# Kernel tuning notes

Measured on AMD Instinct MI355X. Metric: run time of the kernel, lower is better.

Reference implementation:

```python
import jax, jax.numpy as jnp
import numpy as np

# irreps_in  = 128x0 + 64x1   (128 scalars, 64 vectors) -> dim 320
# irreps_out = 128x0 + 64x1 ; irreps_with_gates = (128+64)x0 + 64x1
B = 8192          # batch (nodes)
N0, N1 = 128, 64  # input multiplicities: scalars, vectors
NS, NV = 128, 64  # output scalars, gated vectors (NV gates appended to scalars)

_eps = np.zeros((3, 3, 3), np.float32)
_eps[0, 1, 2] = _eps[1, 2, 0] = _eps[2, 0, 1] = 1.0
_eps[0, 2, 1] = _eps[2, 1, 0] = _eps[1, 0, 2] = -1.0
EPS = jnp.asarray(_eps)  # Levi-Civita, used for the 1x1->1 CG path


def setup_inputs() -> dict:
    key = jax.random.key(0)
    ks = jax.random.split(key, 5)
    x = jax.random.normal(ks[0], (B, N0 + 3 * N1), jnp.float32)
    # fully-connected (uvw) path weights of the tensor square
    w000 = jax.random.normal(ks[1], (N0, N0, NS + NV), jnp.float32)
    w110 = jax.random.normal(ks[2], (N1, N1, NS + NV), jnp.float32)
    w011 = jax.random.normal(ks[3], (N0, N1, NV), jnp.float32)
    w111 = jax.random.normal(ks[4], (N1, N1, NV), jnp.float32)
    return {"x": x, "w000": w000, "w110": w110, "w011": w011, "w111": w111}


def reference(x, w000, w110, w011, w111):
    x0 = x[:, :N0]                        # [B, N0] scalars
    x1 = x[:, N0:].reshape(-1, N1, 3)     # [B, N1, 3] vectors

    inv_sqrt2 = 1.0 / np.sqrt(2.0)

    # ---- tensor square, scalar (l=0) outputs: NS scalars + NV gates ----
    s000 = jnp.einsum('bu,bv,uvw->bw', x0, x0, w000) * (1.0 / N0)
    dots = jnp.einsum('bui,bvi->buv', x1, x1) * (1.0 / np.sqrt(3.0))
    s110 = jnp.einsum('buv,uvw->bw', dots, w110) * (1.0 / N1)
    scalars = (s000 + s110) * inv_sqrt2   # [B, NS+NV], avg over 2 paths

    # ---- tensor square, vector (l=1) outputs: NV vectors ----
    v011 = jnp.einsum('bu,bvi,uvw->bwi', x0, x1, w011) * (1.0 / np.sqrt(N0 * N1))
    v111 = jnp.einsum('ijk,bui,bvj,uvw->bwk', EPS, x1, x1, w111) * (inv_sqrt2 / N1)
    vecs = (v011 + v111) * inv_sqrt2      # [B, NV, 3]

    # ---- e3nn.nn.Gate ----
    s_out = jax.nn.silu(scalars[:, :NS])            # act_scalars on true scalars
    g = jax.nn.sigmoid(scalars[:, NS:])             # act_gates on NV gate scalars
    v_out = vecs * g[:, :, None]                    # gate the non-scalar irreps

    return jnp.concatenate([s_out, v_out.reshape(v_out.shape[0], -1)], axis=1)
```

## Files before the change

### kernel.cpp

```cpp
#include <hip/hip_runtime.h>
#include <cstdint>

static constexpr int B_  = 8192;
static constexpr int NW_ = 192;

typedef __attribute__((ext_vector_type(8))) _Float16 h8v;
typedef __attribute__((ext_vector_type(2))) _Float16 h2v;
typedef __attribute__((ext_vector_type(4))) float f4v;
typedef __attribute__((ext_vector_type(2))) float f2v;
typedef __attribute__((ext_vector_type(4))) unsigned u4v;
typedef __attribute__((ext_vector_type(2))) unsigned u2v;

#define DI __device__ __forceinline__

DI h2v uh(unsigned u) { return __builtin_bit_cast(h2v, u); }
DI unsigned hu(h2v h) { return __builtin_bit_cast(unsigned, h); }
DI h2v hsplat(unsigned short bits) {
  _Float16 v = __builtin_bit_cast(_Float16, bits);
  h2v t; t.x = v; t.y = v; return t;
}
DI unsigned hpack(float lo, float hi) {
  h2v t; t.x = (_Float16)lo; t.y = (_Float16)hi;
  return __builtin_bit_cast(unsigned, t);
}
DI short f2h_bits(float f) { return __builtin_bit_cast(short, (_Float16)f); }

DI f4v mfma16h(h8v a, h8v b, f4v c) {
  return __builtin_amdgcn_mfma_f32_16x16x32_f16(a, b, c, 0, 0, 0);
}

static constexpr unsigned PK_BU0 = 606436u;
static constexpr unsigned PK_BV0 = 1030628u;
static constexpr unsigned PK_BU2 = 4u;
static constexpr unsigned PK_BV2 = 20u;
DI int tab2(unsigned pack, int blk) { return (int)((pack >> (2 * blk)) & 3u); }

__global__ void prep_all(const float* __restrict__ w000, const float* __restrict__ w110,
                         const float* __restrict__ w011, const float* __restrict__ w111,
                         short* __restrict__ wsc, short* __restrict__ wve) {
  __shared__ unsigned short T[32][200];
  const int t = threadIdx.x;
  const int bi = blockIdx.x;
  const float s000 = 1.0f / (128.0f * 1.41421356237f);
  const float s110 = 1.0f / (64.0f * 2.44948974968f);
  const float sv   = 1.0f / 128.0f;

  if (bi < 416) {
    const int s = bi;
    const float* W; int dim; float scale; int blk, ik, bu, bv;
    if (s < 320) {
      blk = s >> 5; ik = s & 31;
      bu = tab2(PK_BU0, blk); bv = tab2(PK_BV0, blk);
      W = w000; dim = 128; scale = s000;
    } else {
      int sp = s - 320; blk = sp >> 5; ik = sp & 31;
      bu = tab2(PK_BU2, blk); bv = tab2(PK_BV2, blk);
      W = w110; dim = 64; scale = s110;
    }
    const int u = bu * 32 + ik;
    const int v = t >> 3, l8 = t & 7;
    float a[24];
    const float* pA = W + ((size_t)(u * dim) + bv * 32 + v) * 192 + l8 * 24;
#pragma unroll
    for (int jj = 0; jj < 6; ++jj) {
      f4v x4 = *(const f4v*)(pA + jj * 4);
      a[jj * 4] = x4.x; a[jj * 4 + 1] = x4.y; a[jj * 4 + 2] = x4.z; a[jj * 4 + 3] = x4.w;
    }
    if (bu != bv) {
      const float* pB = W + ((size_t)((bv * 32 + v)) * dim + u) * 192 + l8 * 24;
#pragma unroll
      for (int jj = 0; jj < 6; ++jj) {
        f4v x4 = *(const f4v*)(pB + jj * 4);
        a[jj * 4] += x4.x; a[jj * 4 + 1] += x4.y; a[jj * 4 + 2] += x4.z; a[jj * 4 + 3] += x4.w;
      }
    }
    unsigned o[12];
#pragma unroll
    for (int i = 0; i < 12; ++i) o[i] = hpack(a[2 * i] * scale, a[2 * i + 1] * scale);
#pragma unroll
    for (int i = 0; i < 3; ++i)
      *(u4v*)(&T[v][l8 * 24 + i * 8]) = u4v{o[4 * i], o[4 * i + 1], o[4 * i + 2], o[4 * i + 3]};
    __syncthreads();
    short* dst = wsc + (size_t)s * 6144;
#pragma unroll
    for (int k = 0; k < 3; ++k) {
      const int unit = t * 3 + k;
      const int F = unit >> 6, lane = unit & 63;
      const int n = F * 16 + (lane & 15);
      const int vr = (lane >> 4) * 8;
      short oo[8];
#pragma unroll
      for (int j = 0; j < 8; ++j) oo[j] = (short)T[vr + j][n];
      *(h8v*)(dst + F * 512 + lane * 8) = *(h8v*)oo;
    }
  } else {
    const int s = bi - 416;
    if (s < 256) {
      const int k32 = t >> 3, l8 = t & 7;
      const float* p = w011 + ((size_t)(s * 32 + k32)) * 64 + l8 * 8;
      f4v x0_ = *(const f4v*)p, x1_ = *(const f4v*)(p + 4);
      u4v o{hpack(x0_.x * sv, x0_.y * sv), hpack(x0_.z * sv, x0_.w * sv),
            hpack(x1_.x * sv, x1_.y * sv), hpack(x1_.z * sv, x1_.w * sv)};
      *(u4v*)(&T[k32][l8 * 8]) = o;
    } else {
      const int sp = s - 256;
      const int blk = sp >> 5, ik = sp & 31;
      const int bu = tab2(PK_BU2, blk), bv = tab2(PK_BV2, blk);
      const int u = bu * 32 + ik;
      const int v = t >> 3, l8 = t & 7;
      float a[8];
      const float* pA = w111 + ((size_t)(u * 64) + bv * 32 + v) * 64 + l8 * 8;
      f4v x0_ = *(const f4v*)pA, x1_ = *(const f4v*)(pA + 4);
      a[0] = x0_.x; a[1] = x0_.y; a[2] = x0_.z; a[3] = x0_.w;
      a[4] = x1_.x; a[5] = x1_.y; a[6] = x1_.z; a[7] = x1_.w;
      if (bu != bv) {
        const float* pB = w111 + ((size_t)((bv * 32 + v)) * 64 + u) * 64 + l8 * 8;
        f4v y0 = *(const f4v*)pB, y1 = *(const f4v*)(pB + 4);
        a[0] -= y0.x; a[1] -= y0.y; a[2] -= y0.z; a[3] -= y0.w;
        a[4] -= y1.x; a[5] -= y1.y; a[6] -= y1.z; a[7] -= y1.w;
      }
      u4v o{hpack(a[0] * sv, a[1] * sv), hpack(a[2] * sv, a[3] * sv),
            hpack(a[4] * sv, a[5] * sv), hpack(a[6] * sv, a[7] * sv)};
      *(u4v*)(&T[v][l8 * 8]) = o;
    }
    __syncthreads();
    const int nf = t >> 6, lane = t & 63;
    const int n = nf * 16 + (lane & 15);
    const int vr = (lane >> 4) * 8;
    short oo[8];
#pragma unroll
    for (int j = 0; j < 8; ++j) oo[j] = (short)T[vr + j][n];
    *(h8v*)(wve + (size_t)s * 2048 + nf * 512 + lane * 8) = *(h8v*)oo;
  }
}

#define X0H_STRIDE 136
#define X1_STRIDE  200

DI void stage_x32w(const float* __restrict__ x, int b0,
                   unsigned short* X0H, unsigned short* X1) {
  const int t = threadIdx.x;
  const int row = t >> 4, l16 = t & 15;
  const float* src = x + (size_t)(b0 + row) * 320;
  f4v v0 = *(const f4v*)(src + l16 * 8);
  f4v v1 = *(const f4v*)(src + l16 * 8 + 4);
  u4v o{hpack(v0.x, v0.y), hpack(v0.z, v0.w), hpack(v1.x, v1.y), hpack(v1.z, v1.w)};
  *(u4v*)(&X0H[row * X0H_STRIDE + l16 * 8]) = o;
  float buf[12];
  f4v a0 = *(const f4v*)(src + 128 + l16 * 12);
  f4v a1 = *(const f4v*)(src + 128 + l16 * 12 + 4);
  f4v a2 = *(const f4v*)(src + 128 + l16 * 12 + 8);
  buf[0] = a0.x; buf[1] = a0.y; buf[2] = a0.z; buf[3] = a0.w;
  buf[4] = a1.x; buf[5] = a1.y; buf[6] = a1.z; buf[7] = a1.w;
  buf[8] = a2.x; buf[9] = a2.y; buf[10] = a2.z; buf[11] = a2.w;
#pragma unroll
  for (int i = 0; i < 3; ++i) {
    u2v w2{hpack(buf[i], buf[3 + i]), hpack(buf[6 + i], buf[9 + i])};
    *(u2v*)(&X1[row * X1_STRIDE + i * 64 + l16 * 4]) = w2;
  }
}

DI void loadB6(h8v* dst, const short* __restrict__ p) {
#pragma unroll
  for (int nf = 0; nf < 6; ++nf) dst[nf] = *(const h8v*)(p + nf * 512);
}
DI void loadB2(h8v* dst, const short* __restrict__ p) {
  dst[0] = *(const h8v*)p;
  dst[1] = *(const h8v*)(p + 512);
}

__global__ __launch_bounds__(512, 2)
void gemm_fused(const float* __restrict__ x, const short* __restrict__ wsc,
                const short* __restrict__ wve, float* __restrict__ out) {
  __shared__ unsigned short X0H[32 * X0H_STRIDE];
  __shared__ unsigned short X1[32 * X1_STRIDE];
  __shared__ f4v dump[4][12][64];
  __shared__ float G[32][64];
  const int b0 = blockIdx.x * 32;

  stage_x32w(x, b0, X0H, X1);
  __syncthreads();

  const int t0 = threadIdx.x;
  const int w = t0 >> 6, lane = t0 & 63;
  const bool isvec = w >= 4;
  const int nh = w & 1, kh = (w >> 1) & 1;
  const int q = lane >> 4, r = lane & 15, q8 = q * 8;

  f4v acc[12];
#pragma unroll
  for (int i = 0; i < 12; ++i) acc[i] = f4v{0.f, 0.f, 0.f, 0.f};

  if (!isvec) {
    const unsigned short* x0f[2];
    const unsigned short* x1f[2];
#pragma unroll
    for (int f = 0; f < 2; ++f) {
      x0f[f] = &X0H[(f * 16 + r) * X0H_STRIDE];
      x1f[f] = &X1[(f * 16 + r) * X1_STRIDE];
    }

    {
      const int s0 = kh * 160;
      const short* wp = wsc + ((size_t)s0 * 12 + nh * 6) * 512 + lane * 8;
      u4v pv[2]; pv[0] = u4v{0, 0, 0, 0}; pv[1] = u4v{0, 0, 0, 0};
      int bu32 = 0;
      h8v b[4][6];
      loadB6(b[0], wp); loadB6(b[1], wp + 6144); loadB6(b[2], wp + 12288);
      for (int t4 = 0; t4 < 40; ++t4) {
#pragma unroll
        for (int uu = 0; uu < 4; ++uu) {
          const int t = t4 * 4 + uu;
          if (t < 157) loadB6(b[(uu + 3) & 3], wp + (size_t)(t + 3) * 6144);
          const int s = s0 + t;
          const int ik = s & 31;
          if (t == 0 || ik == 0) {
            const int blk = s >> 5;
            const int bv32 = tab2(PK_BV0, blk) * 32;
            bu32 = tab2(PK_BU0, blk) * 32;
            pv[0] = *(const u4v*)(x0f[0] + bv32 + q8);
            pv[1] = *(const u4v*)(x0f[1] + bv32 + q8);
          }
          h8v a[2];
#pragma unroll
          for (int f = 0; f < 2; ++f) {
            h2v xu = hsplat(x0f[f][bu32 + ik]);
            u4v pa;
#pragma unroll
            for (int m = 0; m < 4; ++m) pa[m] = hu(uh(pv[f][m]) * xu);
            a[f] = __builtin_bit_cast(h8v, pa);
          }
          __builtin_amdgcn_s_setprio(1);
#pragma unroll
          for (int nf = 0; nf < 6; ++nf)
#pragma unroll
            for (int f = 0; f < 2; ++f)
              acc[f * 6 + nf] = mfma16h(a[f], b[uu & 3][nf], acc[f * 6 + nf]);
          __builtin_amdgcn_s_setprio(0);
        }
      }
    }

    {
      const int sp0 = kh * 48;
      const short* wp = wsc + ((size_t)(320 + sp0) * 12 + nh * 6) * 512 + lane * 8;
      h8v b[4][6];
      loadB6(b[0], wp); loadB6(b[1], wp + 6144); loadB6(b[2], wp + 12288);
      for (int t4 = 0; t4 < 12; ++t4) {
#pragma unroll
        for (int uu = 0; uu < 4; ++uu) {
          const int t = t4 * 4 + uu;
          if (t < 45) loadB6(b[(uu + 3) & 3], wp + (size_t)(t + 3) * 6144);
          const int sp = sp0 + t;
          const int blk = sp >> 5, ik = sp & 31;
          const int bu32 = tab2(PK_BU2, blk) * 32;
          const int bv32 = tab2(PK_BV2, blk) * 32;
          h8v a[2];
#pragma unroll
          for (int f = 0; f < 2; ++f) {
            h2v us0 = hsplat(x1f[f][bu32 + ik]);
            h2v us1 = hsplat(x1f[f][64 + bu32 + ik]);
            h2v us2 = hsplat(x1f[f][128 + bu32 + ik]);
            u4v p0 = *(const u4v*)(x1f[f] + bv32 + q8);
            u4v p1 = *(const u4v*)(x1f[f] + 64 + bv32 + q8);
            u4v p2 = *(const u4v*)(x1f[f] + 128 + bv32 + q8);
            u4v pa;
#pragma unroll
            for (int m = 0; m < 4; ++m) {
              h2v sm = uh(p0[m]) * us0;
              sm = sm + uh(p1[m]) * us1;
              sm = sm + uh(p2[m]) * us2;
              pa[m] = hu(sm);
            }
            a[f] = __builtin_bit_cast(h8v, pa);
          }
          __builtin_amdgcn_s_setprio(1);
#pragma unroll
          for (int nf = 0; nf < 6; ++nf)
#pragma unroll
            for (int f = 0; f < 2; ++f)
              acc[f * 6 + nf] = mfma16h(a[f], b[uu & 3][nf], acc[f * 6 + nf]);
          __builtin_amdgcn_s_setprio(0);
        }
      }
    }
  } else {
    const unsigned short* x0r[2];
    const unsigned short* x1r[2];
#pragma unroll
    for (int ff = 0; ff < 2; ++ff) {
      x0r[ff] = &X0H[(ff * 16 + r) * X0H_STRIDE];
      x1r[ff] = &X1[(ff * 16 + r) * X1_STRIDE];
    }

    {
      const int u0 = kh * 64;
      const short* wp = wve + (size_t)(u0 * 2) * 2048 + nh * 1024 + lane * 8;
      h8v b[4][2];
      loadB2(b[0], wp); loadB2(b[1], wp + 2048); loadB2(b[2], wp + 4096);
      for (int t4 = 0; t4 < 32; ++t4) {
#pragma unroll
        for (int uu = 0; uu < 4; ++uu) {
          const int t = t4 * 4 + uu;
          if (t < 125) loadB2(b[(uu + 3) & 3], wp + (size_t)(t + 3) * 2048);
          const int g = t >> 1, j = t & 1;
          const int vb = j * 32 + q8;
          h8v a[2][3];
#pragma unroll
          for (int ff = 0; ff < 2; ++ff) {
            h2v xu2 = hsplat(x0r[ff][u0 + g]);
#pragma unroll
            for (int i = 0; i < 3; ++i) {
              u4v p = *(const u4v*)(x1r[ff] + i * 64 + vb);
              u4v pa;
#pragma unroll
              for (int m = 0; m < 4; ++m) pa[m] = hu(uh(p[m]) * xu2);
              a[ff][i] = __builtin_bit_cast(h8v, pa);
            }
          }
          __builtin_amdgcn_s_setprio(1);
#pragma unroll
          for (int ip = 0; ip < 3; ++ip)
#pragma unroll
            for (int nfl = 0; nfl < 2; ++nfl)
#pragma unroll
              for (int ff = 0; ff < 2; ++ff)
                acc[(ff * 3 + ip) * 2 + nfl] =
                    mfma16h(a[ff][ip], b[uu & 3][nfl], acc[(ff * 3 + ip) * 2 + nfl]);
          __builtin_amdgcn_s_setprio(0);
        }
      }
    }

    {
      const int sp0 = kh * 48;
      const short* wp = wve + (size_t)(256 + sp0) * 2048 + nh * 1024 + lane * 8;
      h8v b[4][2];
      loadB2(b[0], wp); loadB2(b[1], wp + 2048); loadB2(b[2], wp + 4096);
      for (int t4 = 0; t4 < 12; ++t4) {
#pragma unroll
        for (int uu = 0; uu < 4; ++uu) {
          const int t = t4 * 4 + uu;
          if (t < 45) loadB2(b[(uu + 3) & 3], wp + (size_t)(t + 3) * 2048);
          const int sp = sp0 + t;
          const int blk = sp >> 5, ik = sp & 31;
          const int bu32 = tab2(PK_BU2, blk) * 32;
          const int bv32 = tab2(PK_BV2, blk) * 32;
          h8v a[2][3];
#pragma unroll
          for (int ff = 0; ff < 2; ++ff) {
            h2v us[3];
            u4v p[3];
#pragma unroll
            for (int i = 0; i < 3; ++i) {
              us[i] = hsplat(x1r[ff][i * 64 + bu32 + ik]);
              p[i] = *(const u4v*)(x1r[ff] + i * 64 + bv32 + q8);
            }
#pragma unroll
            for (int ip = 0; ip < 3; ++ip) {
              const int i1 = (ip + 1) % 3, i2 = (ip + 2) % 3;
              u4v pa;
#pragma unroll
              for (int m = 0; m < 4; ++m)
                pa[m] = hu(uh(p[i2][m]) * us[i1] - uh(p[i1][m]) * us[i2]);
              a[ff][ip] = __builtin_bit_cast(h8v, pa);
            }
          }
          __builtin_amdgcn_s_setprio(1);
#pragma unroll
          for (int ip = 0; ip < 3; ++ip)
#pragma unroll
            for (int nfl = 0; nfl < 2; ++nfl)
#pragma unroll
              for (int ff = 0; ff < 2; ++ff)
                acc[(ff * 3 + ip) * 2 + nfl] =
                    mfma16h(a[ff][ip], b[uu & 3][nfl], acc[(ff * 3 + ip) * 2 + nfl]);
          __builtin_amdgcn_s_setprio(0);
        }
      }
    }
  }

  const int slot = (isvec ? 2 : 0) + nh;
  if (kh == 1) {
#pragma unroll
    for (int i = 0; i < 12; ++i) dump[slot][i][lane] = acc[i];
  }
  __syncthreads();

  if (kh == 0 && !isvec) {
#pragma unroll
    for (int f = 0; f < 2; ++f)
#pragma unroll
      for (int nf = 0; nf < 6; ++nf) {
        f4v v = acc[f * 6 + nf] + dump[slot][f * 6 + nf][lane];
        const int n = (nh * 6 + nf) * 16 + r;
#pragma unroll
        for (int reg = 0; reg < 4; ++reg) {
          const int row = f * 16 + q * 4 + reg;
          const float val = v[reg];
          const float sg = 1.0f / (1.0f + __expf(-val));
          if (n < 128) out[(size_t)(b0 + row) * 320 + n] = val * sg;
          else         G[row][n - 128] = sg;
        }
      }
  }
  __syncthreads();

  if (kh == 0 && isvec) {
#pragma unroll
    for (int ff = 0; ff < 2; ++ff)
#pragma unroll
      for (int ip = 0; ip < 3; ++ip)
#pragma unroll
        for (int nfl = 0; nfl < 2; ++nfl) {
          const int ai = (ff * 3 + ip) * 2 + nfl;
          f4v v = acc[ai] + dump[slot][ai][lane];
          const int n = (nh * 2 + nfl) * 16 + r;
#pragma unroll
          for (int reg = 0; reg < 4; ++reg) {
            const int row = ff * 16 + q * 4 + reg;
            out[(size_t)(b0 + row) * 320 + 128 + n * 3 + ip] = v[reg] * G[row][n];
          }
        }
  }
}

extern "C" void kernel_launch(void* const* d_in, const int* in_sizes, int n_in,
                              void* d_out, int out_size, void* d_ws, size_t ws_size,
                              hipStream_t stream) {
  const float* x    = (const float*)d_in[0];
  const float* w000 = (const float*)d_in[1];
  const float* w110 = (const float*)d_in[2];
  const float* w011 = (const float*)d_in[3];
  const float* w111 = (const float*)d_in[4];
  float* out = (float*)d_out;

  char* ws = (char*)d_ws;
  short* wsc = (short*)ws;
  short* wve = (short*)(ws + 5111808);

  prep_all  <<<768, 256, 0, stream>>>(w000, w110, w011, w111, wsc, wve);
  gemm_fused<<<256, 512, 0, stream>>>(x, wsc, wve, out);
}
```

Baseline: 159.0 us.

## Split K four ways across 1024-thread blocks with double-buffered weight loads

Doubles the threads per block from 512 to 1024 so each output tile's K dimension is split across four waves instead of two. A three-stage weight-fragment reduction through two shared-memory dump buffers merges the partial sums. The four-deep register ring of B fragments becomes a two-buffer ping-pong, which cuts register use so the larger block fits. The aim is more waves per CU to hide the latency of streaming weights from global memory, at the cost of an extra barrier, more shared memory, and shallower prefetch.

```diff
diff --git a/kernel.cpp b/kernel.cpp
--- a/kernel.cpp
+++ b/kernel.cpp
@@ -169,22 +169,24 @@
   dst[1] = *(const h8v*)(p + 512);
 }
 
-__global__ __launch_bounds__(512, 2)
+__global__ __launch_bounds__(1024, 4)
 void gemm_fused(const float* __restrict__ x, const short* __restrict__ wsc,
                 const short* __restrict__ wve, float* __restrict__ out) {
   __shared__ unsigned short X0H[32 * X0H_STRIDE];
   __shared__ unsigned short X1[32 * X1_STRIDE];
-  __shared__ f4v dump[4][12][64];
+  __shared__ f4v dumpA[4][12][64];
+  __shared__ f4v dumpB[4][12][64];
   __shared__ float G[32][64];
   const int b0 = blockIdx.x * 32;
 
-  stage_x32w(x, b0, X0H, X1);
+  if (threadIdx.x < 512) stage_x32w(x, b0, X0H, X1);
   __syncthreads();
 
   const int t0 = threadIdx.x;
   const int w = t0 >> 6, lane = t0 & 63;
-  const bool isvec = w >= 4;
-  const int nh = w & 1, kh = (w >> 1) & 1;
+  const bool isvec = w >= 8;
+  const int ww = w & 7;
+  const int nh = ww & 1, kh = ww >> 1;
   const int q = lane >> 4, r = lane & 15, q8 = q * 8;
 
   f4v acc[12];
@@ -201,87 +203,92 @@
     }
 
     {
-      const int s0 = kh * 160;
+      const int s0 = kh * 80;
       const short* wp = wsc + ((size_t)s0 * 12 + nh * 6) * 512 + lane * 8;
       u4v pv[2]; pv[0] = u4v{0, 0, 0, 0}; pv[1] = u4v{0, 0, 0, 0};
       int bu32 = 0;
-      h8v b[4][6];
-      loadB6(b[0], wp); loadB6(b[1], wp + 6144); loadB6(b[2], wp + 12288);
-      for (int t4 = 0; t4 < 40; ++t4) {
-#pragma unroll
-        for (int uu = 0; uu < 4; ++uu) {
-          const int t = t4 * 4 + uu;
-          if (t < 157) loadB6(b[(uu + 3) & 3], wp + (size_t)(t + 3) * 6144);
-          const int s = s0 + t;
-          const int ik = s & 31;
-          if (t == 0 || ik == 0) {
-            const int blk = s >> 5;
-            const int bv32 = tab2(PK_BV0, blk) * 32;
-            bu32 = tab2(PK_BU0, blk) * 32;
-            pv[0] = *(const u4v*)(x0f[0] + bv32 + q8);
-            pv[1] = *(const u4v*)(x0f[1] + bv32 + q8);
+      h8v ba[6], bb[6];
+      loadB6(ba, wp);
+      auto step = [&](int t, const h8v* b) {
+        const int s = s0 + t;
+        const int ik = s & 31;
+        if (t == 0 || ik == 0) {
+          const int blk = s >> 5;
+          const int bv32 = tab2(PK_BV0, blk) * 32;
+          bu32 = tab2(PK_BU0, blk) * 32;
+          pv[0] = *(const u4v*)(x0f[0] + bv32 + q8);
+          pv[1] = *(const u4v*)(x0f[1] + bv32 + q8);
+        }
+        h2v xu0 = hsplat(x0f[0][bu32 + ik]);
+        h2v xu1 = hsplat(x0f[1][bu32 + ik]);
+        u4v pa0, pa1;
+#pragma unroll
+        for (int m = 0; m < 4; ++m) {
+          pa0[m] = hu(uh(pv[0][m]) * xu0);
+          pa1[m] = hu(uh(pv[1][m]) * xu1);
+        }
+        h8v a0 = __builtin_bit_cast(h8v, pa0);
+        h8v a1 = __builtin_bit_cast(h8v, pa1);
+        __builtin_amdgcn_s_setprio(1);
+#pragma unroll
+        for (int nf = 0; nf < 6; ++nf) {
+          acc[nf]     = mfma16h(a0, b[nf], acc[nf]);
+          acc[6 + nf] = mfma16h(a1, b[nf], acc[6 + nf]);
+        }
+        __builtin_amdgcn_s_setprio(0);
+      };
+      for (int t2 = 0; t2 < 40; ++t2) {
+        loadB6(bb, wp + 6144);
+        step(2 * t2, ba);
+        if (t2 != 39) loadB6(ba, wp + 12288);
+        step(2 * t2 + 1, bb);
+        wp += 12288;
+      }
+    }
+
+    {
+      const int sp0 = kh * 24;
+      const short* wp = wsc + ((size_t)(320 + sp0) * 12 + nh * 6) * 512 + lane * 8;
+      h8v ba[6], bb[6];
+      loadB6(ba, wp);
+      auto step = [&](int t, const h8v* b) {
+        const int sp = sp0 + t;
+        const int blk = sp >> 5, ik = sp & 31;
+        const int bu32 = tab2(PK_BU2, blk) * 32;
+        const int bv32 = tab2(PK_BV2, blk) * 32;
+        h8v a[2];
+#pragma unroll
+        for (int f = 0; f < 2; ++f) {
+          h2v us0 = hsplat(x1f[f][bu32 + ik]);
+          h2v us1 = hsplat(x1f[f][64 + bu32 + ik]);
+          h2v us2 = hsplat(x1f[f][128 + bu32 + ik]);
+          u4v p0 = *(const u4v*)(x1f[f] + bv32 + q8);
+          u4v p1 = *(const u4v*)(x1f[f] + 64 + bv32 + q8);
+          u4v p2 = *(const u4v*)(x1f[f] + 128 + bv32 + q8);
+          u4v pa;
+#pragma unroll
+          for (int m = 0; m < 4; ++m) {
+            h2v sm = uh(p0[m]) * us0;
+            sm = sm + uh(p1[m]) * us1;
+            sm = sm + uh(p2[m]) * us2;
+            pa[m] = hu(sm);
           }
-          h8v a[2];
-#pragma unroll
-          for (int f = 0; f < 2; ++f) {
-            h2v xu = hsplat(x0f[f][bu32 + ik]);
-            u4v pa;
-#pragma unroll
-            for (int m = 0; m < 4; ++m) pa[m] = hu(uh(pv[f][m]) * xu);
-            a[f] = __builtin_bit_cast(h8v, pa);
-          }
-          __builtin_amdgcn_s_setprio(1);
-#pragma unroll
-          for (int nf = 0; nf < 6; ++nf)
-#pragma unroll
-            for (int f = 0; f < 2; ++f)
-              acc[f * 6 + nf] = mfma16h(a[f], b[uu & 3][nf], acc[f * 6 + nf]);
-          __builtin_amdgcn_s_setprio(0);
-        }
-      }
-    }
-
-    {
-      const int sp0 = kh * 48;
-      const short* wp = wsc + ((size_t)(320 + sp0) * 12 + nh * 6) * 512 + lane * 8;
-      h8v b[4][6];
-      loadB6(b[0], wp); loadB6(b[1], wp + 6144); loadB6(b[2], wp + 12288);
-      for (int t4 = 0; t4 < 12; ++t4) {
-#pragma unroll
-        for (int uu = 0; uu < 4; ++uu) {
-          const int t = t4 * 4 + uu;
-          if (t < 45) loadB6(b[(uu + 3) & 3], wp + (size_t)(t + 3) * 6144);
-          const int sp = sp0 + t;
-          const int blk = sp >> 5, ik = sp & 31;
-          const int bu32 = tab2(PK_BU2, blk) * 32;
-          const int bv32 = tab2(PK_BV2, blk) * 32;
-          h8v a[2];
-#pragma unroll
-          for (int f = 0; f < 2; ++f) {
-            h2v us0 = hsplat(x1f[f][bu32 + ik]);
-            h2v us1 = hsplat(x1f[f][64 + bu32 + ik]);
-            h2v us2 = hsplat(x1f[f][128 + bu32 + ik]);
-            u4v p0 = *(const u4v*)(x1f[f] + bv32 + q8);
-            u4v p1 = *(const u4v*)(x1f[f] + 64 + bv32 + q8);
-            u4v p2 = *(const u4v*)(x1f[f] + 128 + bv32 + q8);
-            u4v pa;
-#pragma unroll
-            for (int m = 0; m < 4; ++m) {
-              h2v sm = uh(p0[m]) * us0;
-              sm = sm + uh(p1[m]) * us1;
-              sm = sm + uh(p2[m]) * us2;
-              pa[m] = hu(sm);
-            }
-            a[f] = __builtin_bit_cast(h8v, pa);
-          }
-          __builtin_amdgcn_s_setprio(1);
-#pragma unroll
-          for (int nf = 0; nf < 6; ++nf)
-#pragma unroll
-            for (int f = 0; f < 2; ++f)
-              acc[f * 6 + nf] = mfma16h(a[f], b[uu & 3][nf], acc[f * 6 + nf]);
-          __builtin_amdgcn_s_setprio(0);
-        }
+          a[f] = __builtin_bit_cast(h8v, pa);
+        }
+        __builtin_amdgcn_s_setprio(1);
+#pragma unroll
+        for (int nf = 0; nf < 6; ++nf) {
+          acc[nf]     = mfma16h(a[0], b[nf], acc[nf]);
+          acc[6 + nf] = mfma16h(a[1], b[nf], acc[6 + nf]);
+        }
+        __builtin_amdgcn_s_setprio(0);
+      };
+      for (int t2 = 0; t2 < 12; ++t2) {
+        loadB6(bb, wp + 6144);
+        step(2 * t2, ba);
+        if (t2 != 11) loadB6(ba, wp + 12288);
+        step(2 * t2 + 1, bb);
+        wp += 12288;
       }
     }
   } else {
@@ -294,97 +301,110 @@
     }
 
     {
-      const int u0 = kh * 64;
+      const int u0 = kh * 32;
       const short* wp = wve + (size_t)(u0 * 2) * 2048 + nh * 1024 + lane * 8;
-      h8v b[4][2];
-      loadB2(b[0], wp); loadB2(b[1], wp + 2048); loadB2(b[2], wp + 4096);
-      for (int t4 = 0; t4 < 32; ++t4) {
-#pragma unroll
-        for (int uu = 0; uu < 4; ++uu) {
-          const int t = t4 * 4 + uu;
-          if (t < 125) loadB2(b[(uu + 3) & 3], wp + (size_t)(t + 3) * 2048);
-          const int g = t >> 1, j = t & 1;
-          const int vb = j * 32 + q8;
-          h8v a[2][3];
-#pragma unroll
-          for (int ff = 0; ff < 2; ++ff) {
-            h2v xu2 = hsplat(x0r[ff][u0 + g]);
-#pragma unroll
-            for (int i = 0; i < 3; ++i) {
-              u4v p = *(const u4v*)(x1r[ff] + i * 64 + vb);
-              u4v pa;
-#pragma unroll
-              for (int m = 0; m < 4; ++m) pa[m] = hu(uh(p[m]) * xu2);
-              a[ff][i] = __builtin_bit_cast(h8v, pa);
-            }
+      h8v ba[2], bb[2];
+      loadB2(ba, wp);
+      auto vstep = [&](int st, const h8v* b) {
+        const int g = st >> 1, j = st & 1;
+        const int vb = j * 32 + q8;
+        h8v a[2][3];
+#pragma unroll
+        for (int ff = 0; ff < 2; ++ff) {
+          h2v xu2 = hsplat(x0r[ff][u0 + g]);
+#pragma unroll
+          for (int i = 0; i < 3; ++i) {
+            u4v p = *(const u4v*)(x1r[ff] + i * 64 + vb);
+            u4v pa;
+#pragma unroll
+            for (int m = 0; m < 4; ++m) pa[m] = hu(uh(p[m]) * xu2);
+            a[ff][i] = __builtin_bit_cast(h8v, pa);
           }
-          __builtin_amdgcn_s_setprio(1);
-#pragma unroll
-          for (int ip = 0; ip < 3; ++ip)
-#pragma unroll
-            for (int nfl = 0; nfl < 2; ++nfl)
-#pragma unroll
-              for (int ff = 0; ff < 2; ++ff)
-                acc[(ff * 3 + ip) * 2 + nfl] =
-                    mfma16h(a[ff][ip], b[uu & 3][nfl], acc[(ff * 3 + ip) * 2 + nfl]);
-          __builtin_amdgcn_s_setprio(0);
-        }
+        }
+        __builtin_amdgcn_s_setprio(1);
+#pragma unroll
+        for (int ip = 0; ip < 3; ++ip)
+#pragma unroll
+          for (int nfl = 0; nfl < 2; ++nfl)
+#pragma unroll
+            for (int ff = 0; ff < 2; ++ff)
+              acc[(ff * 3 + ip) * 2 + nfl] =
+                  mfma16h(a[ff][ip], b[nfl], acc[(ff * 3 + ip) * 2 + nfl]);
+        __builtin_amdgcn_s_setprio(0);
+      };
+      for (int t2 = 0; t2 < 32; ++t2) {
+        loadB2(bb, wp + 2048);
+        vstep(2 * t2, ba);
+        if (t2 != 31) loadB2(ba, wp + 4096);
+        vstep(2 * t2 + 1, bb);
+        wp += 4096;
       }
     }
 
     {
-      const int sp0 = kh * 48;
+      const int sp0 = kh * 24;
       const short* wp = wve + (size_t)(256 + sp0) * 2048 + nh * 1024 + lane * 8;
-      h8v b[4][2];
-      loadB2(b[0], wp); loadB2(b[1], wp + 2048); loadB2(b[2], wp + 4096);
-      for (int t4 = 0; t4 < 12; ++t4) {
-#pragma unroll
-        for (int uu = 0; uu < 4; ++uu) {
-          const int t = t4 * 4 + uu;
-          if (t < 45) loadB2(b[(uu + 3) & 3], wp + (size_t)(t + 3) * 2048);
-          const int sp = sp0 + t;
-          const int blk = sp >> 5, ik = sp & 31;
-          const int bu32 = tab2(PK_BU2, blk) * 32;
-          const int bv32 = tab2(PK_BV2, blk) * 32;
-          h8v a[2][3];
-#pragma unroll
-          for (int ff = 0; ff < 2; ++ff) {
-            h2v us[3];
-            u4v p[3];
-#pragma unroll
-            for (int i = 0; i < 3; ++i) {
-              us[i] = hsplat(x1r[ff][i * 64 + bu32 + ik]);
-              p[i] = *(const u4v*)(x1r[ff] + i * 64 + bv32 + q8);
-            }
-#pragma unroll
-            for (int ip = 0; ip < 3; ++ip) {
-              const int i1 = (ip + 1) % 3, i2 = (ip + 2) % 3;
-              u4v pa;
-#pragma unroll
-              for (int m = 0; m < 4; ++m)
-                pa[m] = hu(uh(p[i2][m]) * us[i1] - uh(p[i1][m]) * us[i2]);
-              a[ff][ip] = __builtin_bit_cast(h8v, pa);
-            }
+      h8v ba[2], bb[2];
+      loadB2(ba, wp);
+      auto vstep = [&](int t, const h8v* b) {
+        const int sp = sp0 + t;
+        const int blk = sp >> 5, ik = sp & 31;
+        const int bu32 = tab2(PK_BU2, blk) * 32;
+        const int bv32 = tab2(PK_BV2, blk) * 32;
+        h8v a[2][3];
+#pragma unroll
+        for (int ff = 0; ff < 2; ++ff) {
+          h2v us[3];
+          u4v p[3];
+#pragma unroll
+          for (int i = 0; i < 3; ++i) {
+            us[i] = hsplat(x1r[ff][i * 64 + bu32 + ik]);
+            p[i] = *(const u4v*)(x1r[ff] + i * 64 + bv32 + q8);
           }
-          __builtin_amdgcn_s_setprio(1);
-#pragma unroll
-          for (int ip = 0; ip < 3; ++ip)
-#pragma unroll
-            for (int nfl = 0; nfl < 2; ++nfl)
-#pragma unroll
-              for (int ff = 0; ff < 2; ++ff)
-                acc[(ff * 3 + ip) * 2 + nfl] =
-                    mfma16h(a[ff][ip], b[uu & 3][nfl], acc[(ff * 3 + ip) * 2 + nfl]);
-          __builtin_amdgcn_s_setprio(0);
-        }
+#pragma unroll
+          for (int ip = 0; ip < 3; ++ip) {
+            const int i1 = (ip + 1) % 3, i2 = (ip + 2) % 3;
+            u4v pa;
+#pragma unroll
+            for (int m = 0; m < 4; ++m)
+              pa[m] = hu(uh(p[i2][m]) * us[i1] - uh(p[i1][m]) * us[i2]);
+            a[ff][ip] = __builtin_bit_cast(h8v, pa);
+          }
+        }
+        __builtin_amdgcn_s_setprio(1);
+#pragma unroll
+        for (int ip = 0; ip < 3; ++ip)
+#pragma unroll
+          for (int nfl = 0; nfl < 2; ++nfl)
+#pragma unroll
+            for (int ff = 0; ff < 2; ++ff)
+              acc[(ff * 3 + ip) * 2 + nfl] =
+                  mfma16h(a[ff][ip], b[nfl], acc[(ff * 3 + ip) * 2 + nfl]);
+        __builtin_amdgcn_s_setprio(0);
+      };
+      for (int t2 = 0; t2 < 12; ++t2) {
+        loadB2(bb, wp + 2048);
+        vstep(2 * t2, ba);
+        if (t2 != 11) loadB2(ba, wp + 4096);
+        vstep(2 * t2 + 1, bb);
+        wp += 4096;
       }
     }
   }
 
   const int slot = (isvec ? 2 : 0) + nh;
+  if (kh == 3) {
+#pragma unroll
+    for (int i = 0; i < 12; ++i) dumpA[slot][i][lane] = acc[i];
+  } else if (kh == 2) {
+#pragma unroll
+    for (int i = 0; i < 12; ++i) dumpB[slot][i][lane] = acc[i];
+  }
+  __syncthreads();
   if (kh == 1) {
 #pragma unroll
-    for (int i = 0; i < 12; ++i) dump[slot][i][lane] = acc[i];
+    for (int i = 0; i < 12; ++i)
+      dumpA[slot][i][lane] = dumpA[slot][i][lane] + dumpB[slot][i][lane] + acc[i];
   }
   __syncthreads();
 
@@ -393,7 +413,7 @@
     for (int f = 0; f < 2; ++f)
 #pragma unroll
       for (int nf = 0; nf < 6; ++nf) {
-        f4v v = acc[f * 6 + nf] + dump[slot][f * 6 + nf][lane];
+        f4v v = acc[f * 6 + nf] + dumpA[slot][f * 6 + nf][lane];
         const int n = (nh * 6 + nf) * 16 + r;
 #pragma unroll
         for (int reg = 0; reg < 4; ++reg) {
@@ -415,7 +435,7 @@
 #pragma unroll
         for (int nfl = 0; nfl < 2; ++nfl) {
           const int ai = (ff * 3 + ip) * 2 + nfl;
-          f4v v = acc[ai] + dump[slot][ai][lane];
+          f4v v = acc[ai] + dumpA[slot][ai][lane];
           const int n = (nh * 2 + nfl) * 16 + r;
 #pragma unroll
           for (int reg = 0; reg < 4; ++reg) {
@@ -441,5 +461,5 @@
   short* wve = (short*)(ws + 5111808);
 
   prep_all  <<<768, 256, 0, stream>>>(w000, w110, w011, w111, wsc, wve);
-  gemm_fused<<<256, 512, 0, stream>>>(x, wsc, wve, out);
-}
+  gemm_fused<<<256, 1024, 0, stream>>>(x, wsc, wve, out);
+}
```

New measurement: 187.6 us. 1.18x slower.

## Stream scalar-path weights through per-wave LDS ring via global_load_lds

Applied to the files above, without the earlier changes.

Replaces the register-held 4-deep prefetch of scalar-path B fragments with a 5-slot per-wave LDS ring. The ring is filled by async global_load_lds DMA and paced by explicit vmcnt waits, then fragments are read from LDS into two alternating register sets. The goal is to cut VGPR pressure and keep more weight loads in flight to hide global latency. In exchange it adds about 120KB of LDS that aliases the dump/G buffers, which needs an extra barrier and likely limits occupancy to one block per CU despite launch_bounds(512,2).

```diff
diff --git a/kernel.cpp b/kernel.cpp
--- a/kernel.cpp
+++ b/kernel.cpp
@@ -27,6 +27,12 @@
 
 DI f4v mfma16h(h8v a, h8v b, f4v c) {
   return __builtin_amdgcn_mfma_f32_16x16x32_f16(a, b, c, 0, 0, 0);
+}
+
+DI void glds16(const short* g, char* l) {
+  __builtin_amdgcn_global_load_lds(
+      (const __attribute__((address_space(1))) void*)g,
+      (__attribute__((address_space(3))) void*)l, 16, 0, 0);
 }
 
 static constexpr unsigned PK_BU0 = 606436u;
@@ -168,14 +174,24 @@
   dst[0] = *(const h8v*)p;
   dst[1] = *(const h8v*)(p + 512);
 }
+DI void stageB6(const short* wp, char* slot) {
+#pragma unroll
+  for (int nf = 0; nf < 6; ++nf) glds16(wp + nf * 512, slot + nf * 1024);
+}
+DI void readB6(h8v* dst, const char* slot, int lane) {
+#pragma unroll
+  for (int nf = 0; nf < 6; ++nf)
+    dst[nf] = *(const h8v*)(slot + nf * 1024 + lane * 16);
+}
 
 __global__ __launch_bounds__(512, 2)
 void gemm_fused(const float* __restrict__ x, const short* __restrict__ wsc,
                 const short* __restrict__ wve, float* __restrict__ out) {
   __shared__ unsigned short X0H[32 * X0H_STRIDE];
   __shared__ unsigned short X1[32 * X1_STRIDE];
-  __shared__ f4v dump[4][12][64];
-  __shared__ float G[32][64];
+  __shared__ alignas(16) char RING[122880];
+  f4v (*dump)[12][64] = reinterpret_cast<f4v (*)[12][64]>(RING);
+  float (*G)[64] = reinterpret_cast<float (*)[64]>(RING + 49152);
   const int b0 = blockIdx.x * 32;
 
   stage_x32w(x, b0, X0H, X1);
@@ -203,42 +219,66 @@
     {
       const int s0 = kh * 160;
       const short* wp = wsc + ((size_t)s0 * 12 + nh * 6) * 512 + lane * 8;
+      char* ring = RING + w * 30720;
       u4v pv[2]; pv[0] = u4v{0, 0, 0, 0}; pv[1] = u4v{0, 0, 0, 0};
       int bu32 = 0;
-      h8v b[4][6];
-      loadB6(b[0], wp); loadB6(b[1], wp + 6144); loadB6(b[2], wp + 12288);
-      for (int t4 = 0; t4 < 40; ++t4) {
-#pragma unroll
-        for (int uu = 0; uu < 4; ++uu) {
-          const int t = t4 * 4 + uu;
-          if (t < 157) loadB6(b[(uu + 3) & 3], wp + (size_t)(t + 3) * 6144);
-          const int s = s0 + t;
-          const int ik = s & 31;
-          if (t == 0 || ik == 0) {
-            const int blk = s >> 5;
-            const int bv32 = tab2(PK_BV0, blk) * 32;
-            bu32 = tab2(PK_BU0, blk) * 32;
-            pv[0] = *(const u4v*)(x0f[0] + bv32 + q8);
-            pv[1] = *(const u4v*)(x0f[1] + bv32 + q8);
-          }
-          h8v a[2];
-#pragma unroll
-          for (int f = 0; f < 2; ++f) {
-            h2v xu = hsplat(x0f[f][bu32 + ik]);
-            u4v pa;
-#pragma unroll
-            for (int m = 0; m < 4; ++m) pa[m] = hu(uh(pv[f][m]) * xu);
-            a[f] = __builtin_bit_cast(h8v, pa);
-          }
-          __builtin_amdgcn_s_setprio(1);
-#pragma unroll
-          for (int nf = 0; nf < 6; ++nf)
-#pragma unroll
-            for (int f = 0; f < 2; ++f)
-              acc[f * 6 + nf] = mfma16h(a[f], b[uu & 3][nf], acc[f * 6 + nf]);
-          __builtin_amdgcn_s_setprio(0);
-        }
-      }
+      stageB6(wp,          ring);
+      stageB6(wp + 6144,   ring + 6144);
+      stageB6(wp + 12288,  ring + 12288);
+      stageB6(wp + 18432,  ring + 18432);
+      asm volatile("s_waitcnt vmcnt(18)" ::: "memory");
+      h8v ba[6], bb[6];
+      readB6(ba, ring, lane);
+      int rslot = 1, wslot = 4;
+      auto step = [&](int t, const h8v* b) {
+        const int s = s0 + t;
+        const int ik = s & 31;
+        if (t == 0 || ik == 0) {
+          const int blk = s >> 5;
+          const int bv32 = tab2(PK_BV0, blk) * 32;
+          bu32 = tab2(PK_BU0, blk) * 32;
+          pv[0] = *(const u4v*)(x0f[0] + bv32 + q8);
+          pv[1] = *(const u4v*)(x0f[1] + bv32 + q8);
+        }
+        h2v xu0 = hsplat(x0f[0][bu32 + ik]);
+        h2v xu1 = hsplat(x0f[1][bu32 + ik]);
+        u4v pa0, pa1;
+#pragma unroll
+        for (int m = 0; m < 4; ++m) {
+          pa0[m] = hu(uh(pv[0][m]) * xu0);
+          pa1[m] = hu(uh(pv[1][m]) * xu1);
+        }
+        h8v a0 = __builtin_bit_cast(h8v, pa0);
+        h8v a1 = __builtin_bit_cast(h8v, pa1);
+        __builtin_amdgcn_s_setprio(1);
+#pragma unroll
+        for (int nf = 0; nf < 6; ++nf) {
+          acc[nf]     = mfma16h(a0, b[nf], acc[nf]);
+          acc[6 + nf] = mfma16h(a1, b[nf], acc[6 + nf]);
+        }
+        __builtin_amdgcn_s_setprio(0);
+      };
+      for (int t2 = 0; t2 < 80; ++t2) {
+        if (t2 < 78) {
+          stageB6(wp + (size_t)(2 * t2 + 4) * 6144, ring + wslot * 6144);
+          wslot = (wslot == 4) ? 0 : wslot + 1;
+        }
+        asm volatile("s_waitcnt vmcnt(18)" ::: "memory");
+        readB6(bb, ring + rslot * 6144, lane);
+        rslot = (rslot == 4) ? 0 : rslot + 1;
+        step(2 * t2, ba);
+        if (t2 < 78) {
+          stageB6(wp + (size_t)(2 * t2 + 5) * 6144, ring + wslot * 6144);
+          wslot = (wslot == 4) ? 0 : wslot + 1;
+        }
+        asm volatile("s_waitcnt vmcnt(18)" ::: "memory");
+        if (t2 != 79) {
+          readB6(ba, ring + rslot * 6144, lane);
+          rslot = (rslot == 4) ? 0 : rslot + 1;
+        }
+        step(2 * t2 + 1, bb);
+      }
+      asm volatile("s_waitcnt vmcnt(0)" ::: "memory");
     }
 
     {
@@ -276,10 +316,10 @@
           }
           __builtin_amdgcn_s_setprio(1);
 #pragma unroll
-          for (int nf = 0; nf < 6; ++nf)
-#pragma unroll
-            for (int f = 0; f < 2; ++f)
-              acc[f * 6 + nf] = mfma16h(a[f], b[uu & 3][nf], acc[f * 6 + nf]);
+          for (int nf = 0; nf < 6; ++nf) {
+            acc[nf]     = mfma16h(a[0], b[uu & 3][nf], acc[nf]);
+            acc[6 + nf] = mfma16h(a[1], b[uu & 3][nf], acc[6 + nf]);
+          }
           __builtin_amdgcn_s_setprio(0);
         }
       }
@@ -380,6 +420,8 @@
       }
     }
   }
+
+  __syncthreads();
 
   const int slot = (isvec ? 2 : 0) + nh;
   if (kh == 1) {
```

Result: slower. 184.9 us (+16.3%).

## Split K across blocks with 64-row tiles and separate reduce-epilogue kernel

Applied to the files above, without the earlier changes.

Each block now stages 64 rows instead of 32 and processes one K half, with waves splitting M instead of K. Block indices are mapped so blocks sharing a K half land on the same XCD group, which should improve L2 reuse of the weight slices. Partial sums are written to workspace in fp32, and a new reduce kernel adds the two halves and applies silu/sigmoid gating. This removes the in-block LDS reduction but adds a global round-trip of partials (~19MB) and an extra kernel launch.

```diff
diff --git a/kernel.cpp b/kernel.cpp
--- a/kernel.cpp
+++ b/kernel.cpp
@@ -137,26 +137,29 @@
 #define X0H_STRIDE 136
 #define X1_STRIDE  200
 
-DI void stage_x32w(const float* __restrict__ x, int b0,
+DI void stage_x64w(const float* __restrict__ x, int b0,
                    unsigned short* X0H, unsigned short* X1) {
   const int t = threadIdx.x;
-  const int row = t >> 4, l16 = t & 15;
-  const float* src = x + (size_t)(b0 + row) * 320;
-  f4v v0 = *(const f4v*)(src + l16 * 8);
-  f4v v1 = *(const f4v*)(src + l16 * 8 + 4);
-  u4v o{hpack(v0.x, v0.y), hpack(v0.z, v0.w), hpack(v1.x, v1.y), hpack(v1.z, v1.w)};
-  *(u4v*)(&X0H[row * X0H_STRIDE + l16 * 8]) = o;
-  float buf[12];
-  f4v a0 = *(const f4v*)(src + 128 + l16 * 12);
-  f4v a1 = *(const f4v*)(src + 128 + l16 * 12 + 4);
-  f4v a2 = *(const f4v*)(src + 128 + l16 * 12 + 8);
-  buf[0] = a0.x; buf[1] = a0.y; buf[2] = a0.z; buf[3] = a0.w;
-  buf[4] = a1.x; buf[5] = a1.y; buf[6] = a1.z; buf[7] = a1.w;
-  buf[8] = a2.x; buf[9] = a2.y; buf[10] = a2.z; buf[11] = a2.w;
-#pragma unroll
-  for (int i = 0; i < 3; ++i) {
-    u2v w2{hpack(buf[i], buf[3 + i]), hpack(buf[6 + i], buf[9 + i])};
-    *(u2v*)(&X1[row * X1_STRIDE + i * 64 + l16 * 4]) = w2;
+#pragma unroll
+  for (int pass = 0; pass < 2; ++pass) {
+    const int row = pass * 32 + (t >> 4), l16 = t & 15;
+    const float* src = x + (size_t)(b0 + row) * 320;
+    f4v v0 = *(const f4v*)(src + l16 * 8);
+    f4v v1 = *(const f4v*)(src + l16 * 8 + 4);
+    u4v o{hpack(v0.x, v0.y), hpack(v0.z, v0.w), hpack(v1.x, v1.y), hpack(v1.z, v1.w)};
+    *(u4v*)(&X0H[row * X0H_STRIDE + l16 * 8]) = o;
+    float buf[12];
+    f4v a0 = *(const f4v*)(src + 128 + l16 * 12);
+    f4v a1 = *(const f4v*)(src + 128 + l16 * 12 + 4);
+    f4v a2 = *(const f4v*)(src + 128 + l16 * 12 + 8);
+    buf[0] = a0.x; buf[1] = a0.y; buf[2] = a0.z; buf[3] = a0.w;
+    buf[4] = a1.x; buf[5] = a1.y; buf[6] = a1.z; buf[7] = a1.w;
+    buf[8] = a2.x; buf[9] = a2.y; buf[10] = a2.z; buf[11] = a2.w;
+#pragma unroll
+    for (int i = 0; i < 3; ++i) {
+      u2v w2{hpack(buf[i], buf[3 + i]), hpack(buf[6 + i], buf[9 + i])};
+      *(u2v*)(&X1[row * X1_STRIDE + i * 64 + l16 * 4]) = w2;
+    }
   }
 }
 
@@ -170,21 +173,23 @@
 }
 
 __global__ __launch_bounds__(512, 2)
-void gemm_fused(const float* __restrict__ x, const short* __restrict__ wsc,
-                const short* __restrict__ wve, float* __restrict__ out) {
-  __shared__ unsigned short X0H[32 * X0H_STRIDE];
-  __shared__ unsigned short X1[32 * X1_STRIDE];
-  __shared__ f4v dump[4][12][64];
-  __shared__ float G[32][64];
-  const int b0 = blockIdx.x * 32;
-
-  stage_x32w(x, b0, X0H, X1);
+void gemm_split(const float* __restrict__ x, const short* __restrict__ wsc,
+                const short* __restrict__ wve,
+                float* __restrict__ Psc, float* __restrict__ Pve) {
+  __shared__ unsigned short X0H[64 * X0H_STRIDE];
+  __shared__ unsigned short X1[64 * X1_STRIDE];
+  const int xcd = blockIdx.x & 7;
+  const int kb  = xcd >> 2;
+  const int tile = (blockIdx.x >> 3) * 4 + (xcd & 3);
+  const int b0 = tile * 64;
+
+  stage_x64w(x, b0, X0H, X1);
   __syncthreads();
 
   const int t0 = threadIdx.x;
   const int w = t0 >> 6, lane = t0 & 63;
   const bool isvec = w >= 4;
-  const int nh = w & 1, kh = (w >> 1) & 1;
+  const int nh = w & 1, mr = (w >> 1) & 1;
   const int q = lane >> 4, r = lane & 15, q8 = q * 8;
 
   f4v acc[12];
@@ -196,12 +201,12 @@
     const unsigned short* x1f[2];
 #pragma unroll
     for (int f = 0; f < 2; ++f) {
-      x0f[f] = &X0H[(f * 16 + r) * X0H_STRIDE];
-      x1f[f] = &X1[(f * 16 + r) * X1_STRIDE];
+      x0f[f] = &X0H[(mr * 32 + f * 16 + r) * X0H_STRIDE];
+      x1f[f] = &X1[(mr * 32 + f * 16 + r) * X1_STRIDE];
     }
 
     {
-      const int s0 = kh * 160;
+      const int s0 = kb * 160;
       const short* wp = wsc + ((size_t)s0 * 12 + nh * 6) * 512 + lane * 8;
       u4v pv[2]; pv[0] = u4v{0, 0, 0, 0}; pv[1] = u4v{0, 0, 0, 0};
       int bu32 = 0;
@@ -242,7 +247,7 @@
     }
 
     {
-      const int sp0 = kh * 48;
+      const int sp0 = kb * 48;
       const short* wp = wsc + ((size_t)(320 + sp0) * 12 + nh * 6) * 512 + lane * 8;
       h8v b[4][6];
       loadB6(b[0], wp); loadB6(b[1], wp + 6144); loadB6(b[2], wp + 12288);
@@ -284,17 +289,29 @@
         }
       }
     }
+
+#pragma unroll
+    for (int f = 0; f < 2; ++f)
+#pragma unroll
+      for (int nf = 0; nf < 6; ++nf) {
+        const int n = (nh * 6 + nf) * 16 + r;
+#pragma unroll
+        for (int reg = 0; reg < 4; ++reg) {
+          const int row = b0 + mr * 32 + f * 16 + q * 4 + reg;
+          Psc[((size_t)kb * B_ + row) * NW_ + n] = acc[f * 6 + nf][reg];
+        }
+      }
   } else {
     const unsigned short* x0r[2];
     const unsigned short* x1r[2];
 #pragma unroll
     for (int ff = 0; ff < 2; ++ff) {
-      x0r[ff] = &X0H[(ff * 16 + r) * X0H_STRIDE];
-      x1r[ff] = &X1[(ff * 16 + r) * X1_STRIDE];
+      x0r[ff] = &X0H[(mr * 32 + ff * 16 + r) * X0H_STRIDE];
+      x1r[ff] = &X1[(mr * 32 + ff * 16 + r) * X1_STRIDE];
     }
 
     {
-      const int u0 = kh * 64;
+      const int u0 = kb * 64;
       const short* wp = wve + (size_t)(u0 * 2) * 2048 + nh * 1024 + lane * 8;
       h8v b[4][2];
       loadB2(b[0], wp); loadB2(b[1], wp + 2048); loadB2(b[2], wp + 4096);
@@ -333,7 +350,7 @@
     }
 
     {
-      const int sp0 = kh * 48;
+      const int sp0 = kb * 48;
       const short* wp = wve + (size_t)(256 + sp0) * 2048 + nh * 1024 + lane * 8;
       h8v b[4][2];
       loadB2(b[0], wp); loadB2(b[1], wp + 2048); loadB2(b[2], wp + 4096);
@@ -379,35 +396,7 @@
         }
       }
     }
-  }
-
-  const int slot = (isvec ? 2 : 0) + nh;
-  if (kh == 1) {
-#pragma unroll
-    for (int i = 0; i < 12; ++i) dump[slot][i][lane] = acc[i];
-  }
-  __syncthreads();
-
-  if (kh == 0 && !isvec) {
-#pragma unroll
-    for (int f = 0; f < 2; ++f)
-#pragma unroll
-      for (int nf = 0; nf < 6; ++nf) {
-        f4v v = acc[f * 6 + nf] + dump[slot][f * 6 + nf][lane];
-        const int n = (nh * 6 + nf) * 16 + r;
-#pragma unroll
-        for (int reg = 0; reg < 4; ++reg) {
-          const int row = f * 16 + q * 4 + reg;
-          const float val = v[reg];
-          const float sg = 1.0f / (1.0f + __expf(-val));
-          if (n < 128) out[(size_t)(b0 + row) * 320 + n] = val * sg;
-          else         G[row][n - 128] = sg;
-        }
-      }
-  }
-  __syncthreads();
-
-  if (kh == 0 && isvec) {
+
 #pragma unroll
     for (int ff = 0; ff < 2; ++ff)
 #pragma unroll
@@ -415,14 +404,32 @@
 #pragma unroll
         for (int nfl = 0; nfl < 2; ++nfl) {
           const int ai = (ff * 3 + ip) * 2 + nfl;
-          f4v v = acc[ai] + dump[slot][ai][lane];
           const int n = (nh * 2 + nfl) * 16 + r;
 #pragma unroll
           for (int reg = 0; reg < 4; ++reg) {
-            const int row = ff * 16 + q * 4 + reg;
-            out[(size_t)(b0 + row) * 320 + 128 + n * 3 + ip] = v[reg] * G[row][n];
-          }
-        }
+            const int row = b0 + mr * 32 + ff * 16 + q * 4 + reg;
+            Pve[(((size_t)kb * 3 + ip) * B_ + row) * 64 + n] = acc[ai][reg];
+          }
+        }
+  }
+}
+
+__global__ void reduce_ep(const float* __restrict__ Psc, const float* __restrict__ Pve,
+                          float* __restrict__ out) {
+  int t = blockIdx.x * blockDim.x + threadIdx.x;
+  int b = t / NW_, c = t % NW_;
+  float v = Psc[(size_t)b * NW_ + c] + Psc[(size_t)(B_ + b) * NW_ + c];
+  float sg = 1.0f / (1.0f + __expf(-v));
+  if (c < 128) {
+    out[(size_t)b * 320 + c] = v * sg;
+  } else {
+    int w = c - 128;
+#pragma unroll
+    for (int i = 0; i < 3; ++i) {
+      float vv = Pve[((size_t)i * B_ + b) * 64 + w] +
+                 Pve[((size_t)(3 + i) * B_ + b) * 64 + w];
+      out[(size_t)b * 320 + 128 + w * 3 + i] = vv * sg;
+    }
   }
 }
 
@@ -439,7 +446,10 @@
   char* ws = (char*)d_ws;
   short* wsc = (short*)ws;
   short* wve = (short*)(ws + 5111808);
+  float* Psc = (float*)(ws + 6553600);
+  float* Pve = (float*)(ws + 19136512);
 
   prep_all  <<<768, 256, 0, stream>>>(w000, w110, w011, w111, wsc, wve);
-  gemm_fused<<<256, 512, 0, stream>>>(x, wsc, wve, out);
-}
+  gemm_split<<<256, 512, 0, stream>>>(x, wsc, wve, Psc, Pve);
+  reduce_ep <<<6144, 256, 0, stream>>>(Psc, Pve, out);
+}
```

After: 159.5 us (median of 2 runs). Within noise of the previous version (+0.3%).
